# Kernel optimization log

Hardware: AMD Instinct MI355X
Metric: run time of the kernel (lower is better)

The kernel has to match this reference:

```python
import jax, jax.numpy as jnp
from jax import lax
import numpy as np

B, N = 2, 50000
C_IMG, MID, PTS_C, OUT = 256, 128, 64, 128
LVL_SHAPES = [(48, 160), (24, 80), (12, 40)]
H_PAD, W_PAD = 384.0, 1280.0  # img_meta['pad_shape']
BN_EPS = 1e-3


def setup_inputs() -> dict:
    key = jax.random.key(0)
    ks = jax.random.split(key, 16)
    inp = {}
    for l, (h, w) in enumerate(LVL_SHAPES):
        inp[f"img_feats{l}"] = jax.random.normal(ks[l], (B, C_IMG, h, w), jnp.float32)
    # lidar points in front of camera: x in [2,60], y in [-30,30], z in [-2,2]
    u = jax.random.uniform(ks[3], (B, N, 3), jnp.float32)
    lo = jnp.array([2.0, -30.0, -2.0], jnp.float32)
    hi = jnp.array([60.0, 30.0, 2.0], jnp.float32)
    inp["pts"] = lo + (hi - lo) * u
    inp["pts_feats"] = jax.random.normal(ks[4], (B * N, PTS_C), jnp.float32)
    # lidar2img = K @ Tr_lidar_to_cam (KITTI-like intrinsics for 1280x384)
    fx = fy = 720.0; cx = 640.0; cy = 192.0
    K = np.array([[fx, 0, cx, 0], [0, fy, cy, 0], [0, 0, 1, 0], [0, 0, 0, 1]], np.float32)
    Tr = np.eye(4, dtype=np.float32)
    Tr[:3, :3] = np.array([[0, -1, 0], [0, 0, -1], [1, 0, 0]], np.float32)
    Tr[:3, 3] = np.array([0.0, -0.3, 0.0], np.float32)
    l2i = (K @ Tr).astype(np.float32)
    inp["lidar2img"] = jnp.tile(jnp.asarray(l2i)[None], (B, 1, 1))
    angs = np.array([0.08, -0.05], np.float32)  # pcd augmentation yaw per frame
    rots = np.stack([np.array([[np.cos(a), -np.sin(a), 0], [np.sin(a), np.cos(a), 0], [0, 0, 1]], np.float32) for a in angs])
    inp["pcd_rotation"] = jnp.asarray(rots)
    inp["pcd_trans"] = jax.random.normal(ks[5], (B, 3), jnp.float32) * 0.2
    # lateral 3x3 convs (ConvModule with act_cfg=None -> conv+bias only)
    inp["lat_w"] = jax.random.normal(ks[6], (3, MID, C_IMG, 3, 3), jnp.float32) * 0.02
    inp["lat_b"] = jnp.zeros((3, MID), jnp.float32)
    inp["img_w"] = jax.random.normal(ks[7], (OUT, MID * 3), jnp.float32) * 0.05
    inp["img_b"] = jnp.zeros((OUT,), jnp.float32)
    inp["pts_w"] = jax.random.normal(ks[8], (OUT, PTS_C), jnp.float32) * 0.1
    inp["pts_b"] = jnp.zeros((OUT,), jnp.float32)
    inp["img_bn_g"] = jnp.ones((OUT,), jnp.float32)
    inp["img_bn_b"] = jnp.zeros((OUT,), jnp.float32)
    inp["img_bn_m"] = jax.random.normal(ks[9], (OUT,), jnp.float32) * 0.1
    inp["img_bn_v"] = jax.random.uniform(ks[10], (OUT,), jnp.float32, 0.5, 1.5)
    inp["pts_bn_g"] = jnp.ones((OUT,), jnp.float32)
    inp["pts_bn_b"] = jnp.zeros((OUT,), jnp.float32)
    inp["pts_bn_m"] = jax.random.normal(ks[11], (OUT,), jnp.float32) * 0.1
    inp["pts_bn_v"] = jax.random.uniform(ks[12], (OUT,), jnp.float32, 0.5, 1.5)
    return inp


def _bilinear_sample(feat, gx, gy):
    """torch.F.grid_sample(bilinear, zeros padding, align_corners=True).
    feat: [C,H,W]; gx,gy: [N] in [-1,1]. Returns [N,C]."""
    C, H, W = feat.shape
    ix = (gx + 1.0) * 0.5 * (W - 1)
    iy = (gy + 1.0) * 0.5 * (H - 1)
    x0 = jnp.floor(ix)
    y0 = jnp.floor(iy)
    wx1 = ix - x0
    wy1 = iy - y0
    wx0 = 1.0 - wx1
    wy0 = 1.0 - wy1

    def gather(xi, yi):
        valid = (xi >= 0) & (xi <= W - 1) & (yi >= 0) & (yi <= H - 1)
        xc = jnp.clip(xi, 0, W - 1).astype(jnp.int32)
        yc = jnp.clip(yi, 0, H - 1).astype(jnp.int32)
        v = feat[:, yc, xc]  # [C,N]
        return jnp.where(valid[None, :], v, 0.0)

    out = (gather(x0, y0) * (wx0 * wy0)[None]
           + gather(x0 + 1, y0) * (wx1 * wy0)[None]
           + gather(x0, y0 + 1) * (wx0 * wy1)[None]
           + gather(x0 + 1, y0 + 1) * (wx1 * wy1)[None])
    return out.T


def _bn(x, g, b, m, v):
    return (x - m) * (g * lax.rsqrt(v + BN_EPS)) + b


def _forward(img_feats0, img_feats1, img_feats2, pts, pts_feats, lidar2img,
             pcd_rotation, pcd_trans, lat_w, lat_b, img_w, img_b,
             img_bn_g, img_bn_b, img_bn_m, img_bn_v,
             pts_w, pts_b, pts_bn_g, pts_bn_b, pts_bn_m, pts_bn_v):
    dn = ('NCHW', 'OIHW', 'NCHW')
    feats = []
    for l, f in enumerate((img_feats0, img_feats1, img_feats2)):
        y = lax.conv_general_dilated(f, lat_w[l], (1, 1), 'SAME', dimension_numbers=dn)
        feats.append(y + lat_b[l][None, :, None, None])

    def make_grid(p, l2i, rot, tr):
        # pcd_flip=False, pcd_scale_factor=1, img_scale_factor=1, crop_offset=0, img_flip=False
        p = (p - tr) @ jnp.linalg.inv(rot)
        p4 = jnp.concatenate([p, jnp.ones((p.shape[0], 1), p.dtype)], axis=-1)
        pc = p4 @ l2i.T
        z = jnp.clip(pc[:, 2], 1e-5)
        gx = (pc[:, 0] / z) / W_PAD * 2.0 - 1.0
        gy = (pc[:, 1] / z) / H_PAD * 2.0 - 1.0
        return gx, gy

    gx, gy = jax.vmap(make_grid)(pts, lidar2img, pcd_rotation, pcd_trans)  # [B,N] each

    sampled = []
    for f in feats:
        sampled.append(jax.vmap(_bilinear_sample)(f, gx, gy))  # [B,N,MID]
    img_pts = jnp.concatenate(sampled, axis=-1).reshape(-1, MID * 3)  # [B*N, 3*MID]

    img_pre = _bn(img_pts @ img_w.T + img_b, img_bn_g, img_bn_b, img_bn_m, img_bn_v)
    pts_pre = _bn(pts_feats @ pts_w.T + pts_b, pts_bn_g, pts_bn_b, pts_bn_m, pts_bn_v)
    return jax.nn.relu(img_pre + pts_pre)


def reference(img_feats0, img_feats1, img_feats2, pts, pts_feats, lidar2img,
              pcd_rotation, pcd_trans, lat_w, lat_b, img_w, img_b,
              img_bn_g, img_bn_b, img_bn_m, img_bn_v,
              pts_w, pts_b, pts_bn_g, pts_bn_b, pts_bn_m, pts_bn_v):
    return _forward(img_feats0, img_feats1, img_feats2, pts, pts_feats, lidar2img,
                    pcd_rotation, pcd_trans, lat_w, lat_b, img_w, img_b,
                    img_bn_g, img_bn_b, img_bn_m, img_bn_v,
                    pts_w, pts_b, pts_bn_g, pts_bn_b, pts_bn_m, pts_bn_v)
```

## Files before the change

kernel.cpp:

```cpp
#include <hip/hip_runtime.h>
#include <stdint.h>

using u16 = unsigned short;
typedef __attribute__((ext_vector_type(8))) short bf16x8;
typedef __attribute__((ext_vector_type(4))) float f32x4;

#define DEVI static __device__ __forceinline__

constexpr int BATCH  = 2;
constexpr int NPTS   = 50000;
constexpr int TOTPTS = BATCH * NPTS;
constexpr int CIMG   = 256;
constexpr int MIDC   = 128;
constexpr int OUTC   = 128;
constexpr int PTSC   = 64;
constexpr int KIMG   = 384;
constexpr int KTOT   = 448;
constexpr float WPADf = 1280.f, HPADf = 384.f;
constexpr float BNEPS = 1e-3f;

DEVI u16 f2bf(float f) {
  unsigned x = __float_as_uint(f);
  return (u16)((x + 0x7fffu + ((x >> 16) & 1u)) >> 16);
}
DEVI unsigned cvt_pk_bf16(float lo, float hi) {
  unsigned r;
  asm("v_cvt_pk_bf16_f32 %0, %1, %2" : "=v"(r) : "v"(lo), "v"(hi));
  return r;
}
DEVI float blo(unsigned u) { return __uint_as_float(u << 16); }
DEVI float bhi(unsigned u) { return __uint_as_float(u & 0xffff0000u); }

DEVI void gload_lds16(const void* g, void* l) {
  __builtin_amdgcn_global_load_lds(
      (const __attribute__((address_space(1))) void*)g,
      (__attribute__((address_space(3))) void*)l, 16, 0, 0);
}

#define CBAR(N)                                             \
  do {                                                      \
    asm volatile("s_waitcnt vmcnt(" #N ")" ::: "memory");   \
    __builtin_amdgcn_s_barrier();                           \
    __builtin_amdgcn_sched_barrier(0);                      \
  } while (0)

__global__ __launch_bounds__(256) void zero_kernel(uint4* __restrict__ p, int n16) {
  int i = blockIdx.x * 256 + threadIdx.x;
  int stride = gridDim.x * 256;
  for (; i < n16; i += stride) p[i] = uint4{0u, 0u, 0u, 0u};
}

__global__ __launch_bounds__(256) void nchw2nhwc_kernel(
    const float* __restrict__ in, u16* __restrict__ outp, int H, int W) {
  __shared__ float s[64][33];
  const int t  = threadIdx.x;
  const int x0 = blockIdx.x * 32;
  const int y  = blockIdx.y;
  const int b  = blockIdx.z >> 2;
  const int c0 = (blockIdx.z & 3) * 64;
  #pragma unroll
  for (int i = 0; i < 8; ++i) {
    int e = t + i * 256, ci = e >> 5, xi = e & 31;
    float v = 0.f;
    if (x0 + xi < W) v = in[((size_t)(b * CIMG + c0 + ci) * H + y) * W + x0 + xi];
    s[ci][xi] = v;
  }
  __syncthreads();
  const int Wp = W + 2;
  #pragma unroll
  for (int i = 0; i < 8; ++i) {
    int e = t + i * 256, xi = e >> 6, ci = e & 63;
    if (x0 + xi < W)
      outp[((size_t)(b * (H + 2) + y + 1) * Wp + x0 + xi + 1) * CIMG + c0 + ci] =
          f2bf(s[ci][xi]);
  }
}

__global__ __launch_bounds__(256) void prep_kernel(
    const float* __restrict__ img_w, const float* __restrict__ img_b,
    const float* __restrict__ pts_w, const float* __restrict__ pts_b,
    const float* __restrict__ ibg, const float* __restrict__ ibb,
    const float* __restrict__ ibm, const float* __restrict__ ibv,
    const float* __restrict__ pbg, const float* __restrict__ pbb,
    const float* __restrict__ pbm, const float* __restrict__ pbv,
    const float* __restrict__ lat_w,
    u16* __restrict__ wg, u16* __restrict__ wc, float* __restrict__ bias)
{
  int e = blockIdx.x * 256 + threadIdx.x;
  if (e < 57344) {
    int j = e & 7, c = (e >> 3) & 127, s = (e >> 10) & 3, ks = e >> 12;
    int k = ks * 32 + s * 8 + j;
    float s1 = ibg[c] * rsqrtf(ibv[c] + BNEPS);
    float s2 = pbg[c] * rsqrtf(pbv[c] + BNEPS);
    float w = (k < KIMG) ? img_w[c * KIMG + k] * s1
                         : pts_w[c * PTSC + (k - KIMG)] * s2;
    wg[e] = f2bf(w);
    if (e < OUTC) {
      float t1 = ibg[e] * rsqrtf(ibv[e] + BNEPS);
      float t2 = pbg[e] * rsqrtf(pbv[e] + BNEPS);
      bias[e] = (img_b[e] - ibm[e]) * t1 + ibb[e] +
                (pts_b[e] - pbm[e]) * t2 + pbb[e];
    }
  } else if (e < 57344 + 3 * 294912) {
    int q = e - 57344;
    int l = q / 294912, r = q % 294912;
    int j = r & 7, c = (r >> 3) & 127, s = (r >> 10) & 3, ks = r >> 12;
    int k = ks * 32 + s * 8 + j;
    int tap = k >> 8, ic = k & 255;
    float w = lat_w[(((size_t)l * 128 + c) * 256 + ic) * 9 + tap];
    wc[(size_t)l * 294912 + r] = f2bf(w);
  }
}

struct ConvParams {
  int base[4];
  int H[3], W[3], tx[3];
  int poff[3];
  int coff[3];
  int woff[3];
};

__global__ __launch_bounds__(512, 2) void conv_mfma_kernel(
    const u16* __restrict__ pad, const u16* __restrict__ wc,
    const float* __restrict__ lat_b, u16* __restrict__ outbuf, ConvParams P)
{
  __shared__ __attribute__((aligned(16))) u16 sA[6 * 18 * 256];
  __shared__ __attribute__((aligned(16))) u16 sB[3 * 4096];
  const int bid = blockIdx.x;
  const int lvl = (bid >= P.base[1]) + (bid >= P.base[2]);
  const int local = bid - P.base[lvl];
  const int H = P.H[lvl], W = P.W[lvl], tilesx = P.tx[lvl];
  const int nxy = tilesx * (H >> 2);
  const int b = local / nxy;
  const int r = local % nxy;
  const int ty = r / tilesx, tx = r - ty * tilesx;
  const int y0 = ty * 4, x0 = tx * 16;
  const int Wp = W + 2;
  const u16* __restrict__ pin = pad + P.poff[lvl];
  const u16* __restrict__ wl  = wc + P.woff[lvl];
  u16* __restrict__ outp = outbuf + P.coff[lvl];

  const int t = threadIdx.x, l = t & 63, wv = t >> 6;
  const int rp = wv >> 2, ocq = wv & 3;
  const int lr = l & 15, lk = l >> 4;

  auto STAGE = [&](int ks) {
    gload_lds16((const char*)wl + (size_t)ks * 8192 + t * 16,
                (char*)sB + (ks % 3) * 8192 + t * 16);
  };
  STAGE(0); STAGE(1); STAGE(2);

  {
    const int pxi = l >> 5;
    const int bo  = (l & 31) * 16;
    #pragma unroll
    for (int it = 0; it < 7; ++it) {
      const int ch = wv + it * 8;
      if (ch < 54) {
        const int rr2 = ch / 9;
        const int pp  = (ch % 9) * 2;
        const int px  = pp + pxi;
        const u16* src = pin +
            (((size_t)(b * (H + 2) + y0 + rr2) * Wp) + x0 + px) * CIMG + (bo >> 1);
        uint4 v = *(const uint4*)src;
        *(uint4*)((char*)sA + ch * 1024 + pxi * 512 + (bo ^ ((px & 7) << 4))) = v;
      }
    }
  }
  __syncthreads();

  f32x4 acc[2][2] = {};
  bf16x8 Ab[2][2];
  auto loadA = [&](int ks) {
    const int tap = ks >> 3, icc = ks & 7;
    const int ky = tap / 3, kx = tap - ky * 3;
    const int px = lr + kx;
    const int swz = (px & 7) << 4;
    #pragma unroll
    for (int ag = 0; ag < 2; ++ag) {
      const int row = rp * 2 + ag + ky;
      const int ba = (row * 18 + px) * 512 + ((icc * 64 + lk * 16) ^ swz);
      Ab[ks & 1][ag] = *(const bf16x8*)((const char*)sA + ba);
    }
  };
  loadA(0);
  const int bbase = (lk * 128 + ocq * 32 + lr) * 16;

  #pragma unroll
  for (int ks = 0; ks < 72; ++ks) {
    if (ks < 71) loadA(ks + 1);
    const bf16x8 A0 = Ab[ks & 1][0], A1 = Ab[ks & 1][1];
    const char* bb = (const char*)sB + (ks % 3) * 8192 + bbase;
    const bf16x8 B0 = *(const bf16x8*)(bb);
    const bf16x8 B1 = *(const bf16x8*)(bb + 256);
    acc[0][0] = __builtin_amdgcn_mfma_f32_16x16x32_bf16(A0, B0, acc[0][0], 0, 0, 0);
    acc[0][1] = __builtin_amdgcn_mfma_f32_16x16x32_bf16(A0, B1, acc[0][1], 0, 0, 0);
    acc[1][0] = __builtin_amdgcn_mfma_f32_16x16x32_bf16(A1, B0, acc[1][0], 0, 0, 0);
    acc[1][1] = __builtin_amdgcn_mfma_f32_16x16x32_bf16(A1, B1, acc[1][1], 0, 0, 0);
    if (ks < 71) {
      if (ks <= 69) CBAR(1); else CBAR(0);
      if (ks + 3 < 72) STAGE(ks + 3);
    }
  }

  #pragma unroll
  for (int ag = 0; ag < 2; ++ag) {
    const int y = y0 + rp * 2 + ag;
    #pragma unroll
    for (int rr = 0; rr < 4; ++rr) {
      const int x = x0 + lk * 4 + rr;
      if (x < W) {
        const size_t o = ((size_t)(b * H + y) * W + x) * MIDC;
        #pragma unroll
        for (int nf = 0; nf < 2; ++nf) {
          const int oc = ocq * 32 + nf * 16 + lr;
          outp[o + oc] = f2bf(acc[ag][nf][rr] + lat_b[lvl * 128 + oc]);
        }
      }
    }
  }
}

__global__ __launch_bounds__(512, 4) void sample_gemm_kernel(
    const float* __restrict__ pts, const float* __restrict__ l2i,
    const float* __restrict__ rot, const float* __restrict__ trans,
    const u16* __restrict__ cbuf,
    const float* __restrict__ Apts,
    const u16*  __restrict__ wg,
    const float* __restrict__ bias,
    float* __restrict__ outp)
{
  __shared__ __attribute__((aligned(16))) u16  sA[64 * KIMG];
  __shared__ __attribute__((aligned(16))) u16  sB[3 * 4096];
  __shared__ __attribute__((aligned(16))) float sP[192 * 8];
  const int t = threadIdx.x;
  const int row0 = blockIdx.x * 64;
  const int l = t & 63, wv = t >> 6;
  const int rg = wv >> 1, wn = wv & 1;
  const int lr = l & 15, lk = l >> 4;

  auto STAGE = [&](int ks) {
    gload_lds16((const char*)wg + ks * 8192 + t * 16,
                (char*)sB + (ks % 3) * 8192 + t * 16);
  };
  STAGE(0); STAGE(1); STAGE(2);

  const int myrow = min(row0 + rg * 16 + lr, TOTPTS - 1);
  float Pr[2][8];
  #pragma unroll
  for (int s2 = 0; s2 < 2; ++s2) {
    const float* __restrict__ p = Apts + (size_t)myrow * PTSC + s2 * 32 + lk * 8;
    *(float4*)&Pr[s2][0] = *(const float4*)(p);
    *(float4*)&Pr[s2][4] = *(const float4*)(p + 4);
  }

  if (t < 192) {
    const int pt = t & 63, lv = t >> 6;
    const int gpt = min(row0 + pt, TOTPTS - 1);
    const int b = (gpt >= NPTS) ? 1 : 0;
    const float* P = pts + (size_t)gpt * 3;
    const float* T = trans + b * 3;
    const float* R = rot + b * 9;
    const float* L = l2i + b * 16;
    float dx = P[0] - T[0], dy = P[1] - T[1], dz = P[2] - T[2];
    float p0 = dx * R[0] + dy * R[1] + dz * R[2];
    float p1 = dx * R[3] + dy * R[4] + dz * R[5];
    float p2 = dx * R[6] + dy * R[7] + dz * R[8];
    float pc0 = L[0] * p0 + L[1] * p1 + L[2]  * p2 + L[3];
    float pc1 = L[4] * p0 + L[5] * p1 + L[6]  * p2 + L[7];
    float pc2 = L[8] * p0 + L[9] * p1 + L[10] * p2 + L[11];
    float z  = fmaxf(pc2, 1e-5f);
    float gx = pc0 / z / WPADf * 2.f - 1.f;
    float gy = pc1 / z / HPADf * 2.f - 1.f;

    const int Wl = 160 >> lv, Hl = 48 >> lv;
    const float Wm1 = (float)(Wl - 1), Hm1 = (float)(Hl - 1);
    float ix = (gx + 1.f) * 0.5f * Wm1;
    float iy = (gy + 1.f) * 0.5f * Hm1;
    float xf = floorf(ix), yf = floorf(iy);
    float wx1 = ix - xf, wy1 = iy - yf;
    float wx0 = 1.f - wx1, wy0 = 1.f - wy1;
    float ax0 = (xf >= 0.f       && xf <= Wm1)       ? wx0 : 0.f;
    float ax1 = (xf + 1.f >= 0.f && xf + 1.f <= Wm1) ? wx1 : 0.f;
    float ay0 = (yf >= 0.f       && yf <= Hm1)       ? wy0 : 0.f;
    float ay1 = (yf + 1.f >= 0.f && yf + 1.f <= Hm1) ? wy1 : 0.f;
    int xi0 = (int)fminf(fmaxf(xf,       0.f), Wm1);
    int xi1 = (int)fminf(fmaxf(xf + 1.f, 0.f), Wm1);
    int yi0 = (int)fminf(fmaxf(yf,       0.f), Hm1);
    int yi1 = (int)fminf(fmaxf(yf + 1.f, 0.f), Hm1);

    const int foff = (lv == 0) ? 0 : (lv == 1) ? 1966080 : 2457600;
    const int base = (foff + ((b * Hl + yi0) * Wl + xi0) * MIDC) * 2;
    const int dxB  = (xi1 - xi0) * MIDC * 2;
    const int dyB  = (yi1 - yi0) * Wl * MIDC * 2;

    float* pp = sP + (lv * 64 + pt) * 8;
    pp[0] = ax0 * ay0; pp[1] = ax1 * ay0; pp[2] = ax0 * ay1; pp[3] = ax1 * ay1;
    ((int*)pp)[4] = base; ((int*)pp)[5] = dxB; ((int*)pp)[6] = dyB;
  }
  __syncthreads();

  {
    const int lane = t & 15, g = t >> 4;
    uint4 q[3][4];
    float4 wts[3];
    int obyte[3];
    auto issueG = [&](int it) {
      const int s = it % 3;
      const int lv = it >> 1;
      const int pt = (it & 1) * 32 + g;
      const float* __restrict__ pp = sP + (lv * 64 + pt) * 8;
      wts[s] = *(const float4*)pp;
      const int base = ((const int*)pp)[4];
      const int dxB  = ((const int*)pp)[5];
      const int dyB  = ((const int*)pp)[6];
      const char* __restrict__ src = (const char*)cbuf + base + lane * 16;
      q[s][0] = *(const uint4*)(src);
      q[s][1] = *(const uint4*)(src + dxB);
      q[s][2] = *(const uint4*)(src + dyB);
      q[s][3] = *(const uint4*)(src + dxB + dyB);
      const int slot = (lv * 16 + lane) ^ (pt & 7);
      obyte[s] = pt * 768 + slot * 16;
    };
    issueG(0); issueG(1);
    #pragma unroll
    for (int it = 0; it < 6; ++it) {
      if (it + 2 < 6) issueG(it + 2);
      const int s = it % 3;
      const float4 w = wts[s];
      const unsigned* a00 = (const unsigned*)&q[s][0];
      const unsigned* a10 = (const unsigned*)&q[s][1];
      const unsigned* a01 = (const unsigned*)&q[s][2];
      const unsigned* a11 = (const unsigned*)&q[s][3];
      uint4 o;
      unsigned* op = (unsigned*)&o;
      #pragma unroll
      for (int j = 0; j < 4; ++j) {
        float rl = blo(a00[j]) * w.x + blo(a10[j]) * w.y
                 + blo(a01[j]) * w.z + blo(a11[j]) * w.w;
        float rh = bhi(a00[j]) * w.x + bhi(a10[j]) * w.y
                 + bhi(a01[j]) * w.z + bhi(a11[j]) * w.w;
        op[j] = cvt_pk_bf16(rl, rh);
      }
      *(uint4*)((char*)sA + obyte[s]) = o;
    }
  }
  __syncthreads();

  f32x4 acc[4] = {};
  bf16x8 Ab[2];
  const int arow = rg * 16 + lr;
  auto loadA = [&](int ks) {
    const int slot = (ks * 4 + lk) ^ (arow & 7);
    Ab[ks & 1] = *(const bf16x8*)((const char*)sA + arow * 768 + slot * 16);
  };
  loadA(0);
  const int bbase = (lk * 128 + wn * 64 + lr) * 16;

  #pragma unroll
  for (int ks = 0; ks < 14; ++ks) {
    if (ks + 1 < 12) loadA(ks + 1);
    bf16x8 A0;
    if (ks < 12) {
      A0 = Ab[ks & 1];
    } else {
      unsigned* au = (unsigned*)&A0;
      #pragma unroll
      for (int jj = 0; jj < 4; ++jj)
        au[jj] = cvt_pk_bf16(Pr[ks - 12][2 * jj], Pr[ks - 12][2 * jj + 1]);
    }
    const char* bb = (const char*)sB + (ks % 3) * 8192 + bbase;
    const bf16x8 B0 = *(const bf16x8*)(bb);
    const bf16x8 B1 = *(const bf16x8*)(bb + 256);
    const bf16x8 B2 = *(const bf16x8*)(bb + 512);
    const bf16x8 B3 = *(const bf16x8*)(bb + 768);
    acc[0] = __builtin_amdgcn_mfma_f32_16x16x32_bf16(A0, B0, acc[0], 0, 0, 0);
    acc[1] = __builtin_amdgcn_mfma_f32_16x16x32_bf16(A0, B1, acc[1], 0, 0, 0);
    acc[2] = __builtin_amdgcn_mfma_f32_16x16x32_bf16(A0, B2, acc[2], 0, 0, 0);
    acc[3] = __builtin_amdgcn_mfma_f32_16x16x32_bf16(A0, B3, acc[3], 0, 0, 0);
    if (ks < 13) {
      if (ks <= 11) CBAR(1); else CBAR(0);
      if (ks + 3 < 14) STAGE(ks + 3);
    }
  }

  #pragma unroll
  for (int rr = 0; rr < 4; ++rr) {
    const int row = row0 + rg * 16 + lk * 4 + rr;
    if (row < TOTPTS) {
      float* __restrict__ po = outp + (size_t)row * OUTC;
      #pragma unroll
      for (int nf = 0; nf < 4; ++nf) {
        const int col = wn * 64 + nf * 16 + lr;
        po[col] = fmaxf(acc[nf][rr] + bias[col], 0.f);
      }
    }
  }
}

extern "C" void kernel_launch(void* const* d_in, const int* in_sizes, int n_in,
                              void* d_out, int out_size, void* d_ws, size_t ws_size,
                              hipStream_t stream) {
  const float* f0_in  = (const float*)d_in[0];
  const float* f1_in  = (const float*)d_in[1];
  const float* f2_in  = (const float*)d_in[2];
  const float* pts    = (const float*)d_in[3];
  const float* ptsf   = (const float*)d_in[4];
  const float* l2i    = (const float*)d_in[5];
  const float* rot    = (const float*)d_in[6];
  const float* trans  = (const float*)d_in[7];
  const float* lat_w  = (const float*)d_in[8];
  const float* lat_b  = (const float*)d_in[9];
  const float* img_w  = (const float*)d_in[10];
  const float* img_b  = (const float*)d_in[11];
  const float* pts_w  = (const float*)d_in[12];
  const float* pts_b  = (const float*)d_in[13];
  const float* ibg    = (const float*)d_in[14];
  const float* ibbv   = (const float*)d_in[15];
  const float* ibm    = (const float*)d_in[16];
  const float* ibv    = (const float*)d_in[17];
  const float* pbg    = (const float*)d_in[18];
  const float* pbbv   = (const float*)d_in[19];
  const float* pbm    = (const float*)d_in[20];
  const float* pbv    = (const float*)d_in[21];
  float* outp = (float*)d_out;

  uint8_t* ws = (uint8_t*)d_ws;
  const size_t off_wc   = 0;
  const size_t off_wg   = 1769472;
  const size_t off_bias = 1884160;
  const size_t off_c0   = 1884672;
  const size_t off_big  = off_c0 + 3932160 + 983040 + 245760;
  const size_t p0_off = 0;
  const size_t p1_off = 4147200;
  const size_t p2_off = 5238784;

  u16*   wc   = (u16*)(ws + off_wc);
  u16*   wg   = (u16*)(ws + off_wg);
  float* bias = (float*)(ws + off_bias);
  u16*   c0   = (u16*)(ws + off_c0);
  u16*   big  = (u16*)(ws + off_big);

  zero_kernel<<<1024, 256, 0, stream>>>((uint4*)big, (5539840 * 2 + 16384) / 16);

  nchw2nhwc_kernel<<<dim3(5, 48, 8), 256, 0, stream>>>(f0_in, big + p0_off, 48, 160);
  nchw2nhwc_kernel<<<dim3(3, 24, 8), 256, 0, stream>>>(f1_in, big + p1_off, 24, 80);
  nchw2nhwc_kernel<<<dim3(2, 12, 8), 256, 0, stream>>>(f2_in, big + p2_off, 12, 40);

  prep_kernel<<<3680, 256, 0, stream>>>(
      img_w, img_b, pts_w, pts_b, ibg, ibbv, ibm, ibv,
      pbg, pbbv, pbm, pbv, lat_w, wg, wc, bias);

  ConvParams P;
  P.base[0] = 0; P.base[1] = 240; P.base[2] = 300; P.base[3] = 318;
  P.H[0] = 48;  P.H[1] = 24; P.H[2] = 12;
  P.W[0] = 160; P.W[1] = 80; P.W[2] = 40;
  P.tx[0] = 10; P.tx[1] = 5;  P.tx[2] = 3;
  P.poff[0] = (int)p0_off; P.poff[1] = (int)p1_off; P.poff[2] = (int)p2_off;
  P.coff[0] = 0; P.coff[1] = 1966080; P.coff[2] = 2457600;
  P.woff[0] = 0; P.woff[1] = 294912;  P.woff[2] = 589824;
  conv_mfma_kernel<<<318, 512, 0, stream>>>(big, wc, lat_b, c0, P);

  sample_gemm_kernel<<<(TOTPTS + 63) / 64, 512, 0, stream>>>(
      pts, l2i, rot, trans, c0, ptsf, wg, bias, outp);

  (void)in_sizes; (void)n_in; (void)out_size; (void)ws_size;
}
```

Measured before the change: 98.29 us.

## Fuse bilinear gather directly into MFMA A-operand, drop LDS A staging

The sample+GEMM kernel goes from 512 threads to 256. Each wave now owns 16 rows across all 128 output columns (8 accumulators) and gathers and bilinearly blends its A fragments straight into registers each k-step, so the LDS sA buffer and its barrier are gone. The aim is to save LDS capacity, cut LDS write/read traffic and the extra sync, and allow more blocks per CU. The tradeoffs are that each point's corner rows are now gathered by a single wave in 64-byte pieces per k-step rather than whole rows, and register pressure rises with 8 accumulators plus double-buffered gather registers. The B staging is split into two loads per thread and the wait counts are adjusted to match.

```diff
diff --git a/kernel.cpp b/kernel.cpp
--- a/kernel.cpp
+++ b/kernel.cpp
@@ -221,7 +221,7 @@
   }
 }
 
-__global__ __launch_bounds__(512, 4) void sample_gemm_kernel(
+__global__ __launch_bounds__(256, 4) void sample_gemm_kernel(
     const float* __restrict__ pts, const float* __restrict__ l2i,
     const float* __restrict__ rot, const float* __restrict__ trans,
     const u16* __restrict__ cbuf,
@@ -230,18 +230,18 @@
     const float* __restrict__ bias,
     float* __restrict__ outp)
 {
-  __shared__ __attribute__((aligned(16))) u16  sA[64 * KIMG];
   __shared__ __attribute__((aligned(16))) u16  sB[3 * 4096];
   __shared__ __attribute__((aligned(16))) float sP[192 * 8];
   const int t = threadIdx.x;
   const int row0 = blockIdx.x * 64;
-  const int l = t & 63, wv = t >> 6;
-  const int rg = wv >> 1, wn = wv & 1;
+  const int l = t & 63, rg = t >> 6;
   const int lr = l & 15, lk = l >> 4;
 
   auto STAGE = [&](int ks) {
-    gload_lds16((const char*)wg + ks * 8192 + t * 16,
-                (char*)sB + (ks % 3) * 8192 + t * 16);
+    const char* src = (const char*)wg + ks * 8192 + t * 16;
+    char* dst = (char*)sB + (ks % 3) * 8192 + t * 16;
+    gload_lds16(src, dst);
+    gload_lds16(src + 4096, dst + 4096);
   };
   STAGE(0); STAGE(1); STAGE(2);
 
@@ -300,86 +300,62 @@
   }
   __syncthreads();
 
-  {
-    const int lane = t & 15, g = t >> 4;
-    uint4 q[3][4];
-    float4 wts[3];
-    int obyte[3];
-    auto issueG = [&](int it) {
-      const int s = it % 3;
-      const int lv = it >> 1;
-      const int pt = (it & 1) * 32 + g;
-      const float* __restrict__ pp = sP + (lv * 64 + pt) * 8;
-      wts[s] = *(const float4*)pp;
-      const int base = ((const int*)pp)[4];
-      const int dxB  = ((const int*)pp)[5];
-      const int dyB  = ((const int*)pp)[6];
-      const char* __restrict__ src = (const char*)cbuf + base + lane * 16;
-      q[s][0] = *(const uint4*)(src);
-      q[s][1] = *(const uint4*)(src + dxB);
-      q[s][2] = *(const uint4*)(src + dyB);
-      q[s][3] = *(const uint4*)(src + dxB + dyB);
-      const int slot = (lv * 16 + lane) ^ (pt & 7);
-      obyte[s] = pt * 768 + slot * 16;
-    };
-    issueG(0); issueG(1);
-    #pragma unroll
-    for (int it = 0; it < 6; ++it) {
-      if (it + 2 < 6) issueG(it + 2);
-      const int s = it % 3;
-      const float4 w = wts[s];
-      const unsigned* a00 = (const unsigned*)&q[s][0];
-      const unsigned* a10 = (const unsigned*)&q[s][1];
-      const unsigned* a01 = (const unsigned*)&q[s][2];
-      const unsigned* a11 = (const unsigned*)&q[s][3];
-      uint4 o;
-      unsigned* op = (unsigned*)&o;
+  f32x4 acc[8] = {};
+  uint4  tq[2][4];
+  float4 wts[2];
+  const int prow = rg * 16 + lr;
+
+  auto issueT = [&](int ks) {
+    const int lv = ks >> 2, ksl = ks & 3;
+    const float* __restrict__ pp = sP + (lv * 64 + prow) * 8;
+    wts[ks & 1] = *(const float4*)pp;
+    const int* ip = (const int*)pp;
+    const char* __restrict__ src =
+        (const char*)cbuf + ip[4] + ksl * 64 + lk * 16;
+    const int dxB = ip[5], dyB = ip[6];
+    tq[ks & 1][0] = *(const uint4*)(src);
+    tq[ks & 1][1] = *(const uint4*)(src + dxB);
+    tq[ks & 1][2] = *(const uint4*)(src + dyB);
+    tq[ks & 1][3] = *(const uint4*)(src + dxB + dyB);
+  };
+  issueT(0);
+
+  const int bbase = (lk * 128 + lr) * 16;
+
+  #pragma unroll
+  for (int ks = 0; ks < 14; ++ks) {
+    if (ks + 1 < 12) issueT(ks + 1);
+    bf16x8 A0;
+    unsigned* au = (unsigned*)&A0;
+    if (ks < 12) {
+      const float4 w = wts[ks & 1];
+      const unsigned* a00 = (const unsigned*)&tq[ks & 1][0];
+      const unsigned* a10 = (const unsigned*)&tq[ks & 1][1];
+      const unsigned* a01 = (const unsigned*)&tq[ks & 1][2];
+      const unsigned* a11 = (const unsigned*)&tq[ks & 1][3];
       #pragma unroll
-      for (int j = 0; j < 4; ++j) {
-        float rl = blo(a00[j]) * w.x + blo(a10[j]) * w.y
-                 + blo(a01[j]) * w.z + blo(a11[j]) * w.w;
-        float rh = bhi(a00[j]) * w.x + bhi(a10[j]) * w.y
-                 + bhi(a01[j]) * w.z + bhi(a11[j]) * w.w;
-        op[j] = cvt_pk_bf16(rl, rh);
+      for (int jj = 0; jj < 4; ++jj) {
+        float rl = blo(a00[jj]) * w.x + blo(a10[jj]) * w.y
+                 + blo(a01[jj]) * w.z + blo(a11[jj]) * w.w;
+        float rh = bhi(a00[jj]) * w.x + bhi(a10[jj]) * w.y
+                 + bhi(a01[jj]) * w.z + bhi(a11[jj]) * w.w;
+        au[jj] = cvt_pk_bf16(rl, rh);
       }
-      *(uint4*)((char*)sA + obyte[s]) = o;
-    }
-  }
-  __syncthreads();
-
-  f32x4 acc[4] = {};
-  bf16x8 Ab[2];
-  const int arow = rg * 16 + lr;
-  auto loadA = [&](int ks) {
-    const int slot = (ks * 4 + lk) ^ (arow & 7);
-    Ab[ks & 1] = *(const bf16x8*)((const char*)sA + arow * 768 + slot * 16);
-  };
-  loadA(0);
-  const int bbase = (lk * 128 + wn * 64 + lr) * 16;
-
-  #pragma unroll
-  for (int ks = 0; ks < 14; ++ks) {
-    if (ks + 1 < 12) loadA(ks + 1);
-    bf16x8 A0;
-    if (ks < 12) {
-      A0 = Ab[ks & 1];
     } else {
-      unsigned* au = (unsigned*)&A0;
       #pragma unroll
       for (int jj = 0; jj < 4; ++jj)
         au[jj] = cvt_pk_bf16(Pr[ks - 12][2 * jj], Pr[ks - 12][2 * jj + 1]);
     }
     const char* bb = (const char*)sB + (ks % 3) * 8192 + bbase;
-    const bf16x8 B0 = *(const bf16x8*)(bb);
-    const bf16x8 B1 = *(const bf16x8*)(bb + 256);
-    const bf16x8 B2 = *(const bf16x8*)(bb + 512);
-    const bf16x8 B3 = *(const bf16x8*)(bb + 768);
-    acc[0] = __builtin_amdgcn_mfma_f32_16x16x32_bf16(A0, B0, acc[0], 0, 0, 0);
-    acc[1] = __builtin_amdgcn_mfma_f32_16x16x32_bf16(A0, B1, acc[1], 0, 0, 0);
-    acc[2] = __builtin_amdgcn_mfma_f32_16x16x32_bf16(A0, B2, acc[2], 0, 0, 0);
-    acc[3] = __builtin_amdgcn_mfma_f32_16x16x32_bf16(A0, B3, acc[3], 0, 0, 0);
+    #pragma unroll
+    for (int nf = 0; nf < 8; ++nf) {
+      const bf16x8 Bn = *(const bf16x8*)(bb + nf * 256);
+      acc[nf] = __builtin_amdgcn_mfma_f32_16x16x32_bf16(A0, Bn, acc[nf], 0, 0, 0);
+    }
     if (ks < 13) {
-      if (ks <= 11) CBAR(1); else CBAR(0);
+      if (ks <= 10) CBAR(6);
+      else if (ks == 11) CBAR(2);
+      else CBAR(0);
       if (ks + 3 < 14) STAGE(ks + 3);
     }
   }
@@ -390,8 +366,8 @@
     if (row < TOTPTS) {
       float* __restrict__ po = outp + (size_t)row * OUTC;
       #pragma unroll
-      for (int nf = 0; nf < 4; ++nf) {
-        const int col = wn * 64 + nf * 16 + lr;
+      for (int nf = 0; nf < 8; ++nf) {
+        const int col = nf * 16 + lr;
         po[col] = fmaxf(acc[nf][rr] + bias[col], 0.f);
       }
     }
@@ -461,7 +437,7 @@
   P.woff[0] = 0; P.woff[1] = 294912;  P.woff[2] = 589824;
   conv_mfma_kernel<<<318, 512, 0, stream>>>(big, wc, lat_b, c0, P);
 
-  sample_gemm_kernel<<<(TOTPTS + 63) / 64, 512, 0, stream>>>(
+  sample_gemm_kernel<<<(TOTPTS + 63) / 64, 256, 0, stream>>>(
       pts, l2i, rot, trans, c0, ptsf, wg, bias, outp);
 
   (void)in_sizes; (void)n_in; (void)out_size; (void)ws_size;
```

Result: slower. 113.7 us (+15.7%).
